# Kernel optimization log

Hardware: AMD Instinct MI355X
Metric: run time of the kernel (lower is better)

Reference implementation:

```python
import jax, jax.numpy as jnp
import numpy as np

COMPRESSION = 2

def setup_inputs() -> dict:
    key = jax.random.key(0)
    k = jax.random.split(key, 5)
    B, H, W, C, Ci = 8, 56, 56, 256, 128
    return {
        "x": jax.random.normal(k[0], (B, H, W, C), dtype=jnp.float32),
        "w_theta": jax.random.normal(k[1], (C, Ci), dtype=jnp.float32) * (2.0 / C) ** 0.5,
        "w_phi": jax.random.normal(k[2], (C, Ci), dtype=jnp.float32) * (2.0 / C) ** 0.5,
        "w_g": jax.random.normal(k[3], (C, Ci), dtype=jnp.float32) * (2.0 / C) ** 0.5,
        "w_final": jax.random.normal(k[4], (Ci, C), dtype=jnp.float32) * (2.0 / Ci) ** 0.5,
    }

def _maxpool1d(z, pool):
    # z: [B, N, Ci]; non-overlapping max pool along N (Keras MaxPool1D default stride=pool)
    B, N, Ci = z.shape
    return z[:, : (N // pool) * pool].reshape(B, N // pool, pool, Ci).max(axis=2)

def reference(x, w_theta, w_phi, w_g, w_final):
    B, H, W, C = x.shape
    Ci = w_theta.shape[1]
    N = H * W
    xf = x.reshape(B, N, C)
    # 1x1 convs == per-position matmuls
    theta = xf @ w_theta                      # [B, N, Ci]
    phi = _maxpool1d(xf @ w_phi, COMPRESSION)  # [B, N/2, Ci]
    g = _maxpool1d(xf @ w_g, COMPRESSION)      # [B, N/2, Ci]
    f = jnp.einsum('bnc,bmc->bnm', theta, phi)  # [B, N, N/2]
    f = jax.nn.softmax(f, axis=-1)
    y = jnp.einsum('bnm,bmc->bnc', f, g)        # [B, N, Ci]
    z = y @ w_final                              # [B, N, C]
    return x + z.reshape(B, H, W, C)
```

## Files before the change

kernel.cpp:

```cpp
#include <hip/hip_runtime.h>

typedef _Float16 f16x8 __attribute__((ext_vector_type(8)));
typedef _Float16 f16x4 __attribute__((ext_vector_type(4)));
typedef short s16x4 __attribute__((ext_vector_type(4)));
typedef float f32x4 __attribute__((ext_vector_type(4)));

#define MFMA_K32(a, b, c) __builtin_amdgcn_mfma_f32_16x16x32_f16(a, b, c, 0, 0, 0)
#define MFMA_BF(a, b, c)  __builtin_amdgcn_mfma_f32_16x16x16bf16_1k(a, b, c, 0, 0, 0)
#define MFMA_F16(a, b, c) __builtin_amdgcn_mfma_f32_16x16x16f16(a, b, c, 0, 0, 0)


__device__ __forceinline__ f16x8 ld8f(const float* __restrict__ p) {
    f32x4 a = *(const f32x4*)p;
    f32x4 b = *(const f32x4*)(p + 4);
    f16x8 r;
    r[0] = (_Float16)a[0]; r[1] = (_Float16)a[1];
    r[2] = (_Float16)a[2]; r[3] = (_Float16)a[3];
    r[4] = (_Float16)b[0]; r[5] = (_Float16)b[1];
    r[6] = (_Float16)b[2]; r[7] = (_Float16)b[3];
    return r;
}
__device__ __forceinline__ unsigned f2bf_rne(float f) {
    unsigned u = __float_as_uint(f);
    return (u + 0x7FFFu + ((u >> 16) & 1u)) >> 16;
}
__device__ __forceinline__ int bfpack_rtz(float lo, float hi) {
    return (int)((__float_as_uint(hi) & 0xFFFF0000u) | (__float_as_uint(lo) >> 16));
}
__device__ __forceinline__ void gl_lds16(const _Float16* g, _Float16* l) {
    __builtin_amdgcn_global_load_lds(
        (const __attribute__((address_space(1))) unsigned*)g,
        (__attribute__((address_space(3))) unsigned*)l, 16, 0, 0);
}

__global__ __launch_bounds__(256) void k_prep(
    const float* __restrict__ wt, const float* __restrict__ wp,
    const float* __restrict__ wg, const float* __restrict__ wf,
    _Float16* __restrict__ wt_f, _Float16* __restrict__ wfT_f) {
    int i = blockIdx.x * 256 + threadIdx.x;
    if (i < 12288) {
        int w    = i >> 12;
        int rem  = i & 4095;
        int ctkc = rem >> 6;
        int l    = rem & 63;
        const float* src = (w == 0) ? wt : (w == 1) ? wp : wg;
        const float* s = src + ((ctkc & 7) * 32 + (l >> 4) * 8) * 128
                             + (ctkc >> 3) * 16 + (l & 15);
        f16x8 v;
#pragma unroll
        for (int jj = 0; jj < 8; ++jj) v[jj] = (_Float16)s[jj * 128];
        *(f16x8*)(wt_f + i * 8) = v;
    } else {
        int j    = i - 12288;
        int ct   = j >> 8;
        int rem  = j & 255;
        int qt   = rem >> 2;
        int kc2e = rem & 3;
        int col  = ct * 16 + (qt & 15);
        int qq   = qt >> 4;
        f16x8 v;
#pragma unroll
        for (int jp = 0; jp < 8; ++jp) {
            int Ci = (kc2e * 2 + (jp >> 2)) * 16 + qq * 4 + (jp & 3);
            v[jp] = (_Float16)wf[Ci * 256 + col];
        }
        *(f16x8*)(wfT_f + j * 8) = v;
    }
}

__global__ __launch_bounds__(256) void k_proj(
    const float* __restrict__ x,
    const _Float16* __restrict__ wt_f,
    _Float16* __restrict__ theta_f,
    _Float16* __restrict__ phi_f,
    short* __restrict__ g_f)
{
    const int w    = blockIdx.y;
    const int wave = threadIdx.x >> 6;
    const int lane = threadIdx.x & 63;
    const int q = lane >> 4, t = lane & 15;
    const int tt = blockIdx.x * 4 + wave;

    __shared__ __align__(16) _Float16 Wl[32768];
    {
        const _Float16* src = wt_f + w * 32768;
#pragma unroll
        for (int j = 0; j < 16; ++j) {
            const int o8 = (j * 256 + threadIdx.x) * 8;
            *(f16x8*)(Wl + o8) = *(const f16x8*)(src + o8);
        }
    }
    __syncthreads();

    const int mrow = tt * 16 + t;
    f16x8 af[8];
#pragma unroll
    for (int kc = 0; kc < 8; ++kc)
        af[kc] = ld8f(x + mrow * 256 + kc * 32 + q * 8);

    const f32x4 zero = {0.f, 0.f, 0.f, 0.f};
    f32x4 acc[8];
#pragma unroll
    for (int ct = 0; ct < 8; ++ct) acc[ct] = zero;

    if (w == 2) {
#pragma unroll
        for (int ct = 0; ct < 8; ++ct) {
            const _Float16* Wc = Wl + (ct * 8) * 512 + lane * 8;
#pragma unroll
            for (int kc = 0; kc < 8; ++kc)
                acc[ct] = MFMA_K32(af[kc], *(const f16x8*)(Wc + kc * 512), acc[ct]);
        }
    } else {
#pragma unroll
        for (int ct = 0; ct < 8; ++ct) {
            const _Float16* Wc = Wl + (ct * 8) * 512 + lane * 8;
#pragma unroll
            for (int kc = 0; kc < 8; ++kc)
                acc[ct] = MFMA_K32(*(const f16x8*)(Wc + kc * 512), af[kc], acc[ct]);
        }
    }

    if (w == 0) {
        _Float16* tb = theta_f + tt * 2048;
#pragma unroll
        for (int ct = 0; ct < 8; ++ct) {
            f16x4 v;
#pragma unroll
            for (int r = 0; r < 4; ++r) v[r] = (_Float16)acc[ct][r];
            const int off = (ct >> 1) * 512
                          + (((ct & 1) * 2 + (q >> 1)) * 16 + t) * 8 + 4 * (q & 1);
            *(f16x4*)(tb + off) = v;
        }
        return;
    }

    const int b     = tt / 196;
    const int tl    = tt - b * 196;
    const int chunk = tl >> 2;
    const int sub   = tl & 3;

    if (w == 1) {
        _Float16* pcb = phi_f + (b * 49 + chunk) * 4096;
#pragma unroll
        for (int ct = 0; ct < 8; ++ct) {
            f32x4 pm;
#pragma unroll
            for (int r = 0; r < 4; ++r)
                pm[r] = fmaxf(acc[ct][r], __shfl_xor(acc[ct][r], 1));
            if (!(t & 1)) {
                f16x4 v;
#pragma unroll
                for (int r = 0; r < 4; ++r) v[r] = (_Float16)pm[r];
                const int off = ((sub >> 1) * 4 + (ct >> 1)) * 512
                              + ((((ct & 1) * 2 + (q >> 1)) * 16)
                                 + (sub & 1) * 8 + (t >> 1)) * 8 + 4 * (q & 1);
                *(f16x4*)(pcb + off) = v;
            }
        }
    } else {
        const int h   = sub >> 1;
        short* gcb = g_f + (b * 49 + chunk) * 4096;
        const int qv  = (sub & 1) * 2 + (q >> 1);
        const int jj0 = (q & 1) * 2;
#pragma unroll
        for (int ct = 0; ct < 8; ++ct) {
            unsigned lo = f2bf_rne(fmaxf(acc[ct][0], acc[ct][1]));
            unsigned hi = f2bf_rne(fmaxf(acc[ct][2], acc[ct][3]));
            *(unsigned*)(gcb + (ct * 2 + h) * 256 + (qv * 16 + t) * 4 + jj0) = lo | (hi << 16);
        }
    }
}

__global__ __launch_bounds__(256) void k_attn(
    const _Float16* __restrict__ theta_f,
    const _Float16* __restrict__ phi_f,
    const short* __restrict__ g_f,
    const _Float16* __restrict__ wfT_f,
    const float* __restrict__ x,
    float* __restrict__ out)
{
    const int blk  = blockIdx.x;
    const int b    = blk & 7;
    const int blkm = blk >> 3;
    const int wave = threadIdx.x >> 6;
    const int lane = threadIdx.x & 63;
    const int q = lane >> 4, t = lane & 15;
    const int m = wave >> 1;
    const int h = wave & 1;

    __shared__ __align__(16) _Float16 kv[2][8192];
    __shared__ float lred[2][64];

    const int tIdx0 = b * 196 + blkm * 2;
    const _Float16* ph = phi_f + b * 200704;
    const _Float16* gt = (const _Float16*)(g_f + b * 200704);

    f16x8 qf[4];
#pragma unroll
    for (int kc = 0; kc < 4; ++kc)
        qf[kc] = *(const f16x8*)(theta_f + (tIdx0 + m) * 2048 + kc * 512 + lane * 8);

    const f32x4 zero = {0.f, 0.f, 0.f, 0.f};
    f32x4 o[8];
#pragma unroll
    for (int ct = 0; ct < 8; ++ct) o[ct] = zero;
    float lsum = 0.f;
    const float L2E = 1.44269504f, SHIFT = 104.0f;

    const _Float16* src0 = (wave < 2) ? (ph + wave * 2048) : (gt + (wave - 2) * 2048);
    const int doff = wave * 2048;

#pragma unroll
    for (int j = 0; j < 4; ++j)
        gl_lds16(src0 + j * 512 + lane * 8, &kv[0][doff + j * 512]);
    __syncthreads();

#pragma unroll 1
    for (int i = 0; i < 49; ++i) {
        if (i + 1 < 49) {
            const _Float16* s = src0 + (i + 1) * 4096;
            _Float16* d = &kv[(i + 1) & 1][doff];
#pragma unroll
            for (int j = 0; j < 4; ++j)
                gl_lds16(s + j * 512 + lane * 8, d + j * 512);
        }

        const _Float16* buf = &kv[i & 1][0];
        f32x4 st = zero;
        __builtin_amdgcn_s_setprio(1);
#pragma unroll
        for (int kc = 0; kc < 4; ++kc) {
            f16x8 a = *(const f16x8*)(buf + (h * 4 + kc) * 512 + lane * 8);
            st = MFMA_K32(a, qf[kc], st);
        }
        __builtin_amdgcn_s_setprio(0);

        f32x4 pv;
#pragma unroll
        for (int r = 0; r < 4; ++r)
            pv[r] = exp2f(st[r] * L2E - SHIFT);
        lsum += (pv[0] + pv[1]) + (pv[2] + pv[3]);
        union { int i2[2]; s16x4 v; } u;
        u.i2[0] = bfpack_rtz(pv[0], pv[1]);
        u.i2[1] = bfpack_rtz(pv[2], pv[3]);

        __builtin_amdgcn_s_setprio(1);
#pragma unroll
        for (int ct = 0; ct < 8; ++ct) {
            s16x4 vf = *(const s16x4*)(buf + 4096 + (ct * 2 + h) * 256 + lane * 4);
            o[ct] = MFMA_BF(vf, u.v, o[ct]);
        }
        __builtin_amdgcn_s_setprio(0);

        __syncthreads();
    }

    float* cb = (float*)&kv[0][0];
    if (h == 1) {
#pragma unroll
        for (int ct = 0; ct < 8; ++ct)
            *(f32x4*)&cb[m * 2048 + ct * 256 + lane * 4] = o[ct];
        lred[m][lane] = lsum;
    }
    __syncthreads();
    if (h == 0) {
#pragma unroll
        for (int ct = 0; ct < 8; ++ct)
            o[ct] += *(const f32x4*)&cb[m * 2048 + ct * 256 + lane * 4];
        lsum += lred[m][lane];
#pragma unroll
        for (int ct = 0; ct < 8; ++ct)
            *(f32x4*)&cb[m * 2048 + ct * 256 + lane * 4] = o[ct];
        lred[m][lane] = lsum;
    }
    __syncthreads();
    if (h == 1) {
#pragma unroll
        for (int ct = 0; ct < 8; ++ct)
            o[ct] = *(const f32x4*)&cb[m * 2048 + ct * 256 + lane * 4];
        lsum = lred[m][lane];
    }

    float lf = lsum;
    lf += __shfl_xor(lf, 16);
    lf += __shfl_xor(lf, 32);
    const float inv = 1.0f / lf;

    f16x4 yf[8];
#pragma unroll
    for (int ct = 0; ct < 8; ++ct)
#pragma unroll
        for (int r = 0; r < 4; ++r)
            yf[ct][r] = (_Float16)(o[ct][r] * inv);

    const int row = (tIdx0 + m) * 16 + t;
#pragma unroll 2
    for (int ci = 0; ci < 8; ++ci) {
        const int ctile = h * 8 + ci;
        union { f16x8 v8; f16x4 v4[2]; } w[4];
#pragma unroll
        for (int pp = 0; pp < 4; ++pp)
            w[pp].v8 = *(const f16x8*)(wfT_f + ctile * 2048 + lane * 32 + pp * 8);
        f32x4 acc = zero;
#pragma unroll
        for (int kc2 = 0; kc2 < 8; ++kc2)
            acc = MFMA_F16(w[kc2 >> 1].v4[kc2 & 1], yf[kc2], acc);
        const int col = ctile * 16 + q * 4;
        f32x4 xv = *(const f32x4*)(x + row * 256 + col);
        *(f32x4*)(out + row * 256 + col) = acc + xv;
    }
}

extern "C" void kernel_launch(void* const* d_in, const int* in_sizes, int n_in,
                              void* d_out, int out_size, void* d_ws, size_t ws_size,
                              hipStream_t stream) {
    const float* x  = (const float*)d_in[0];
    const float* wt = (const float*)d_in[1];
    const float* wp = (const float*)d_in[2];
    const float* wg = (const float*)d_in[3];
    const float* wf = (const float*)d_in[4];
    float* out = (float*)d_out;

    _Float16* ws      = (_Float16*)d_ws;
    _Float16* wt_f    = ws;
    _Float16* wfT_f   = ws + 98304;
    _Float16* theta_f = ws + 131072;
    _Float16* phi_f   = ws + 3342336;
    short*    g_f     = (short*)(ws + 4947968);

    k_prep<<<dim3(64),     256, 0, stream>>>(wt, wp, wg, wf, wt_f, wfT_f);
    k_proj<<<dim3(392, 3), 256, 0, stream>>>(x, wt_f, theta_f, phi_f, g_f);
    k_attn<<<dim3(784),    256, 0, stream>>>(theta_f, phi_f, g_f, wfT_f, x, out);
}
```

Before: 155.4 us.

## Deepen attention K/V LDS pipeline to four buffers with explicit vmcnt waits

Replaces the double-buffered LDS prefetch of phi/g tiles in the attention kernel with a 4-slot ring that keeps two tiles in flight ahead of compute. Each iteration waits with s_waitcnt vmcnt on only the oldest load and uses a raw s_barrier instead of __syncthreads, so global-to-LDS latency is hidden deeper. LDS use doubles to 64KB per block, which may lower occupancy. Reusing a slot two iterations after it was read relies on the barrier ordering.

```diff
diff --git a/kernel.cpp b/kernel.cpp
--- a/kernel.cpp
+++ b/kernel.cpp
@@ -171,6 +171,34 @@
         }
     }
 }
+
+#define ISSUE(c) { const _Float16* s_ = src0 + (c) * 4096; \
+    _Float16* d_ = &kv[(c) & 3][doff]; \
+    _Pragma("unroll") for (int j = 0; j < 4; ++j) \
+        gl_lds16(s_ + j * 512 + lane * 8, d_ + j * 512); }
+
+#define COMPUTE(i) { \
+    const _Float16* buf = &kv[(i) & 3][0]; \
+    f32x4 st = zero; \
+    __builtin_amdgcn_s_setprio(1); \
+    _Pragma("unroll") for (int kc = 0; kc < 4; ++kc) { \
+        f16x8 a = *(const f16x8*)(buf + (h * 4 + kc) * 512 + lane * 8); \
+        st = MFMA_K32(a, qf[kc], st); \
+    } \
+    __builtin_amdgcn_s_setprio(0); \
+    f32x4 pv; \
+    _Pragma("unroll") for (int r = 0; r < 4; ++r) \
+        pv[r] = exp2f(st[r] * L2E - SHIFT); \
+    lsum += (pv[0] + pv[1]) + (pv[2] + pv[3]); \
+    union { int i2[2]; s16x4 v; } u; \
+    u.i2[0] = bfpack_rtz(pv[0], pv[1]); \
+    u.i2[1] = bfpack_rtz(pv[2], pv[3]); \
+    __builtin_amdgcn_s_setprio(1); \
+    _Pragma("unroll") for (int ct = 0; ct < 8; ++ct) { \
+        s16x4 vf = *(const s16x4*)(buf + 4096 + (ct * 2 + h) * 256 + lane * 4); \
+        o[ct] = MFMA_BF(vf, u.v, o[ct]); \
+    } \
+    __builtin_amdgcn_s_setprio(0); }
 
 __global__ __launch_bounds__(256) void k_attn(
     const _Float16* __restrict__ theta_f,
@@ -189,7 +217,7 @@
     const int m = wave >> 1;
     const int h = wave & 1;
 
-    __shared__ __align__(16) _Float16 kv[2][8192];
+    __shared__ __align__(16) _Float16 kv[4][8192];
     __shared__ float lred[2][64];
 
     const int tIdx0 = b * 196 + blkm * 2;
@@ -211,50 +239,23 @@
     const _Float16* src0 = (wave < 2) ? (ph + wave * 2048) : (gt + (wave - 2) * 2048);
     const int doff = wave * 2048;
 
-#pragma unroll
-    for (int j = 0; j < 4; ++j)
-        gl_lds16(src0 + j * 512 + lane * 8, &kv[0][doff + j * 512]);
+    ISSUE(0);
+    ISSUE(1);
+
+#pragma unroll 1
+    for (int i = 0; i < 47; ++i) {
+        ISSUE(i + 2);
+        asm volatile("s_waitcnt vmcnt(8)" ::: "memory");
+        __builtin_amdgcn_s_barrier();
+        COMPUTE(i);
+    }
+    asm volatile("s_waitcnt vmcnt(4)" ::: "memory");
+    __builtin_amdgcn_s_barrier();
+    COMPUTE(47);
+    asm volatile("s_waitcnt vmcnt(0)" ::: "memory");
+    __builtin_amdgcn_s_barrier();
+    COMPUTE(48);
     __syncthreads();
-
-#pragma unroll 1
-    for (int i = 0; i < 49; ++i) {
-        if (i + 1 < 49) {
-            const _Float16* s = src0 + (i + 1) * 4096;
-            _Float16* d = &kv[(i + 1) & 1][doff];
-#pragma unroll
-            for (int j = 0; j < 4; ++j)
-                gl_lds16(s + j * 512 + lane * 8, d + j * 512);
-        }
-
-        const _Float16* buf = &kv[i & 1][0];
-        f32x4 st = zero;
-        __builtin_amdgcn_s_setprio(1);
-#pragma unroll
-        for (int kc = 0; kc < 4; ++kc) {
-            f16x8 a = *(const f16x8*)(buf + (h * 4 + kc) * 512 + lane * 8);
-            st = MFMA_K32(a, qf[kc], st);
-        }
-        __builtin_amdgcn_s_setprio(0);
-
-        f32x4 pv;
-#pragma unroll
-        for (int r = 0; r < 4; ++r)
-            pv[r] = exp2f(st[r] * L2E - SHIFT);
-        lsum += (pv[0] + pv[1]) + (pv[2] + pv[3]);
-        union { int i2[2]; s16x4 v; } u;
-        u.i2[0] = bfpack_rtz(pv[0], pv[1]);
-        u.i2[1] = bfpack_rtz(pv[2], pv[3]);
-
-        __builtin_amdgcn_s_setprio(1);
-#pragma unroll
-        for (int ct = 0; ct < 8; ++ct) {
-            s16x4 vf = *(const s16x4*)(buf + 4096 + (ct * 2 + h) * 256 + lane * 4);
-            o[ct] = MFMA_BF(vf, u.v, o[ct]);
-        }
-        __builtin_amdgcn_s_setprio(0);
-
-        __syncthreads();
-    }
 
     float* cb = (float*)&kv[0][0];
     if (h == 1) {
```

New measurement: 175.3 us. 1.13x slower.
